# Kernel tuning notes

Measured on AMD Instinct MI355X. Metric: run time of the kernel, lower is better.

Reference implementation:

```python
import jax, jax.numpy as jnp
import numpy as np

L = 16          # n_levels
F = 2           # n_features_per_level
LOG2_T = 19
T = 1 << LOG2_T # hashmap size per level
BASE_RES = 16
FINEST_RES = 2048
_b = (FINEST_RES / BASE_RES) ** (1.0 / (L - 1))
RES = [int(np.floor(BASE_RES * _b ** l)) for l in range(L)]
PRIMES = (1, 2654435761, 805459861, 3674653429)
H = 2 * L * F   # 64 = n_neurons (static 32 + dynamic 32)
N_PTS = 2097152


def hash_encode(coords, table):
    """Multi-resolution hash grid encoding. coords [N,D] in [0,1], table [L,T,F] -> [N, L*F]."""
    N, D = coords.shape
    # 2^D corner offsets of the enclosing grid cell
    offsets = np.stack(
        np.meshgrid(*([np.array([0, 1], dtype=np.uint32)] * D), indexing='ij'), -1
    ).reshape(-1, D)
    primes = [jnp.uint32(p) for p in PRIMES[:D]]
    feats = []
    for l in range(L):  # fixed small loop over levels
        pos = coords * RES[l]
        grid = jnp.floor(pos)
        frac = pos - grid                       # [N,D] interpolation weights
        gu = grid.astype(jnp.int32).astype(jnp.uint32)
        acc = jnp.zeros((N, F), coords.dtype)
        for off in offsets:                     # fixed 2^D corners
            idx = gu + off[None, :]
            h = idx[:, 0] * primes[0]
            for d in range(1, D):
                h = h ^ (idx[:, d] * primes[d])
            h = (h & jnp.uint32(T - 1)).astype(jnp.int32)
            w = jnp.prod(jnp.where(off[None, :] != 0, frac, 1.0 - frac), axis=1)
            acc = acc + w[:, None] * table[l, h]
        feats.append(acc)
    return jnp.concatenate(feats, -1)


def setup_inputs() -> dict:
    key = jax.random.key(0)
    ks = jax.random.split(key, 12)
    s = 1.0 / np.sqrt(H)
    return {
        'x': jax.random.uniform(ks[0], (N_PTS, 3), jnp.float32),
        't': jax.random.uniform(ks[1], (), jnp.float32),
        'table_static': jax.random.uniform(ks[2], (L, T, F), jnp.float32, -1e-4, 1e-4),
        'table_dynamic': jax.random.uniform(ks[3], (L, T, F), jnp.float32, -1e-4, 1e-4),
        'w1_0': jax.random.normal(ks[4], (H, H), jnp.float32) * s,
        'w1_1': jax.random.normal(ks[5], (H, H), jnp.float32) * s,
        'w1_2': jax.random.normal(ks[6], (H, H), jnp.float32) * s,
        'w2_0': jax.random.normal(ks[7], (H, H), jnp.float32) * s,
        'w2_1': jax.random.normal(ks[8], (H, H), jnp.float32) * s,
        'w2_2': jax.random.normal(ks[9], (H, 1), jnp.float32) * s,
        'skip_alpha': jnp.float32(0.5),
    }


def reference(x, t, table_static, table_dynamic, w1_0, w1_1, w1_2,
              w2_0, w2_1, w2_2, skip_alpha):
    relu = jax.nn.relu
    # t_input = cat([x, full((N,1), t)])
    t_col = jnp.broadcast_to(t.astype(x.dtype), (x.shape[0], 1))
    t_input = jnp.concatenate([x, t_col], axis=1)
    static_features = hash_encode(x, table_static)          # [N,32]
    dynamic_features = hash_encode(t_input, table_dynamic)  # [N,32]
    feat = jnp.concatenate([static_features, dynamic_features], -1)  # [N,64]
    # net_1: 2 hidden layers, ReLU everywhere incl. output activation
    h = relu(feat @ w1_0)
    h = relu(h @ w1_1)
    out1 = relu(h @ w1_2)
    # adaptive skip blend
    blend = out1 * skip_alpha + (1.0 - skip_alpha) * feat
    # net_2: 2 hidden layers ReLU, linear output -> [N,1]
    h = relu(blend @ w2_0)
    h = relu(h @ w2_1)
    return h @ w2_2
```

## Files before the change

kernel.cpp:

```cpp
#include <hip/hip_runtime.h>
#include <math.h>

#define LVLS 16
#define TMASK ((1u << 19) - 1u)
#define NT 256
#define TSLICE (1u << 20)
#define KPL (1u << 19)

typedef _Float16 h4 __attribute__((ext_vector_type(4)));
typedef short bf8i __attribute__((ext_vector_type(8)));
typedef float f4 __attribute__((ext_vector_type(4)));

#define ESCALE 1024.0f
#define EINV   0.0009765625f

struct ResParams { float rf[LVLS]; };

__device__ __forceinline__ unsigned hash3(unsigned ux, unsigned uy, unsigned uz) {
    return ux ^ (uy * 2654435761u) ^ (uz * 805459861u);
}

__device__ __forceinline__ unsigned short bf16_rne(float f) {
    unsigned u = __builtin_bit_cast(unsigned, f);
    unsigned r = (u + 0x7FFFu + ((u >> 16) & 1u)) >> 16;
    return (unsigned short)r;
}
__device__ __forceinline__ float bf16_to_f(unsigned short h) {
    unsigned u = ((unsigned)h) << 16;
    return __builtin_bit_cast(float, u);
}
__device__ __forceinline__ void split8(const float* v, bf8i& h, bf8i& l) {
    #pragma unroll
    for (int j = 0; j < 8; ++j) {
        unsigned short hb = bf16_rne(v[j]);
        h[j] = (short)hb;
        l[j] = (short)bf16_rne(v[j] - bf16_to_f(hb));
    }
}

__global__ __launch_bounds__(NT, 8)
void build_E(const float* __restrict__ tabs, const float* __restrict__ tabd,
             const float* __restrict__ t_ptr, h4* __restrict__ E, ResParams rp)
{
    const unsigned idx = blockIdx.x * NT + threadIdx.x;
    const unsigned l = idx >> 19;
    const unsigned k = idx & TMASK;
    const float r = rp.rf[l];
    const float tt = t_ptr[0];
    const float ft = tt * r;
    const float gt = floorf(ft);
    const float wt = ft - gt;
    const unsigned ut = (unsigned)(int)gt;
    const unsigned c0 = (ut * 3674653429u) & TMASK;
    const unsigned c1 = ((ut + 1u) * 3674653429u) & TMASK;
    const float* ts = tabs + (size_t)l * TSLICE;
    const float* td = tabd + (size_t)l * TSLICE;
    const float2 s  = *(const float2*)(ts + (size_t)k * 2u);
    const float2 d0 = *(const float2*)(td + (size_t)(k ^ c0) * 2u);
    const float2 d1 = *(const float2*)(td + (size_t)(k ^ c1) * 2u);
    const float om = 1.f - wt;
    h4 v;
    v.x = (_Float16)(s.x * ESCALE);
    v.y = (_Float16)(s.y * ESCALE);
    v.z = (_Float16)((om * d0.x + wt * d1.x) * ESCALE);
    v.w = (_Float16)((om * d0.y + wt * d1.y) * ESCALE);
    E[idx] = v;
}

__global__ __launch_bounds__(NT)
void build_W(const float* __restrict__ w10, const float* __restrict__ w11,
             const float* __restrict__ w12, const float* __restrict__ w20,
             const float* __restrict__ w21, const float* __restrict__ w22,
             unsigned short* __restrict__ Wf)
{
    const int tid = blockIdx.x * NT + threadIdx.x;
    if (tid >= 6 * 4 * 2 * 64) return;
    const int lane = tid & 63;
    const int ks = (tid >> 6) & 1;
    const int nt = (tid >> 7) & 3;
    const int L  = tid >> 9;
    const int g = lane >> 4, c = lane & 15;
    unsigned short* dst = Wf + (size_t)tid * 16;
    #pragma unroll
    for (int j = 0; j < 8; ++j) {
        const int k = ks * 32 + g * 8 + j;
        float v;
        if      (L == 0) v = w10[k * 64 + nt * 16 + c];
        else if (L == 1) v = w11[k * 64 + nt * 16 + c];
        else if (L == 2) v = w12[k * 64 + nt * 16 + c];
        else if (L == 3) v = w20[k * 64 + nt * 16 + c];
        else if (L == 4) v = w21[k * 64 + nt * 16 + c];
        else             v = (nt == 0 && c == 0) ? w22[k] : 0.f;
        unsigned short hb = bf16_rne(v);
        unsigned short lb = bf16_rne(v - bf16_to_f(hb));
        dst[j]     = hb;
        dst[8 + j] = lb;
    }
}

__global__ __launch_bounds__(NT, 8)
void enc_all(const float* __restrict__ x, const h4* __restrict__ E,
             h4* __restrict__ fb, long cp, int npts, ResParams rp)
{
    const int l = blockIdx.y;
    const int gid = blockIdx.x * NT + threadIdx.x;
    if (gid >= npts) return;
    const float r = rp.rf[l];
    const h4* Es = E + (size_t)l * KPL;

    const float px = x[3 * gid + 0];
    const float py = x[3 * gid + 1];
    const float pz = x[3 * gid + 2];
    const float fx = px * r, fy = py * r, fz = pz * r;
    const float gx = floorf(fx), gy = floorf(fy), gz = floorf(fz);
    const float wx = fx - gx, wy = fy - gy, wz = fz - gz;
    const unsigned ux = (unsigned)(int)gx;
    const unsigned uy = (unsigned)(int)gy;
    const unsigned uz = (unsigned)(int)gz;
    float a0 = 0.f, a1 = 0.f, b0 = 0.f, b1 = 0.f;
    #pragma unroll
    for (int cc = 0; cc < 8; ++cc) {
        const unsigned ox = (cc >> 2) & 1, oy = (cc >> 1) & 1, oz = cc & 1;
        const unsigned kk = hash3(ux + ox, uy + oy, uz + oz) & TMASK;
        const float w = (ox ? wx : 1.f - wx)
                      * (oy ? wy : 1.f - wy)
                      * (oz ? wz : 1.f - wz);
        const h4 e = Es[kk];
        a0 = fmaf(w, (float)e.x, a0);
        a1 = fmaf(w, (float)e.y, a1);
        b0 = fmaf(w, (float)e.z, b0);
        b1 = fmaf(w, (float)e.w, b1);
    }
    h4 v;
    v.x = (_Float16)a0;
    v.y = (_Float16)a1;
    v.z = (_Float16)b0;
    v.w = (_Float16)b1;
    __builtin_nontemporal_store(__builtin_bit_cast(unsigned long long, v),
                                (unsigned long long*)&fb[(size_t)l * cp + gid]);
}

#define MLPT 128
__global__ __launch_bounds__(MLPT)
void mlp_mfma(const h4* __restrict__ fb, long cp, const uint4* __restrict__ Wf,
              const float* __restrict__ alpha_ptr, float* __restrict__ out, int npts)
{
    __shared__ float XBs[2][64 * 68];
    const int lane = threadIdx.x & 63;
    const int wv   = threadIdx.x >> 6;
    const int base = blockIdx.x * MLPT + wv * 64;
    if (base >= npts) return;
    float* xb = XBs[wv];
    const int g = lane >> 4, c = lane & 15;
    const float alpha = alpha_ptr[0];
    const float oma = 1.f - alpha;

    bf8i ah[4][2], al[4][2];

    #pragma unroll
    for (int mt = 0; mt < 4; ++mt) {
        float t0[8], t1[8];
        #pragma unroll
        for (int jj = 0; jj < 4; ++jj) {
            const h4 e = fb[(size_t)(g * 4 + jj) * cp + base + mt * 16 + c];
            t0[2 * jj] = (float)e.x; t0[2 * jj + 1] = (float)e.y;
            t1[2 * jj] = (float)e.z; t1[2 * jj + 1] = (float)e.w;
        }
        split8(t0, ah[mt][0], al[mt][0]);
        split8(t1, ah[mt][1], al[mt][1]);
    }

    auto run_layer = [&](int Lidx, bool relu) {
        #pragma unroll
        for (int nt = 0; nt < 4; ++nt) {
            const uint4* wp0 = Wf + ((size_t)(((Lidx * 4 + nt) * 2 + 0) * 64 + lane)) * 2;
            const uint4* wp1 = Wf + ((size_t)(((Lidx * 4 + nt) * 2 + 1) * 64 + lane)) * 2;
            const bf8i wh0 = __builtin_bit_cast(bf8i, wp0[0]);
            const bf8i wl0 = __builtin_bit_cast(bf8i, wp0[1]);
            const bf8i wh1 = __builtin_bit_cast(bf8i, wp1[0]);
            const bf8i wl1 = __builtin_bit_cast(bf8i, wp1[1]);
            f4 acc[4];
            #pragma unroll
            for (int mt = 0; mt < 4; ++mt) acc[mt] = (f4){0.f, 0.f, 0.f, 0.f};
            #pragma unroll
            for (int mt = 0; mt < 4; ++mt)
                acc[mt] = __builtin_amdgcn_mfma_f32_16x16x32_bf16(ah[mt][0], wh0, acc[mt], 0, 0, 0);
            #pragma unroll
            for (int mt = 0; mt < 4; ++mt)
                acc[mt] = __builtin_amdgcn_mfma_f32_16x16x32_bf16(ah[mt][1], wh1, acc[mt], 0, 0, 0);
            #pragma unroll
            for (int mt = 0; mt < 4; ++mt)
                acc[mt] = __builtin_amdgcn_mfma_f32_16x16x32_bf16(ah[mt][0], wl0, acc[mt], 0, 0, 0);
            #pragma unroll
            for (int mt = 0; mt < 4; ++mt)
                acc[mt] = __builtin_amdgcn_mfma_f32_16x16x32_bf16(ah[mt][1], wl1, acc[mt], 0, 0, 0);
            #pragma unroll
            for (int mt = 0; mt < 4; ++mt)
                acc[mt] = __builtin_amdgcn_mfma_f32_16x16x32_bf16(al[mt][0], wh0, acc[mt], 0, 0, 0);
            #pragma unroll
            for (int mt = 0; mt < 4; ++mt)
                acc[mt] = __builtin_amdgcn_mfma_f32_16x16x32_bf16(al[mt][1], wh1, acc[mt], 0, 0, 0);
            #pragma unroll
            for (int mt = 0; mt < 4; ++mt)
              #pragma unroll
              for (int r = 0; r < 4; ++r) {
                float v = acc[mt][r];
                if (relu) v = fmaxf(v, 0.f);
                xb[(mt * 16 + g * 4 + r) * 68 + nt * 16 + c] = v;
              }
        }
    };

    auto load_frags = [&](bool blend) {
        asm volatile("s_waitcnt lgkmcnt(0)" ::: "memory");
        #pragma unroll
        for (int mt = 0; mt < 4; ++mt) {
            float t0[8], t1[8];
            #pragma unroll
            for (int j = 0; j < 8; ++j) t0[j] = xb[(mt * 16 + c) * 68 + g * 8 + j];
            #pragma unroll
            for (int j = 0; j < 8; ++j) t1[j] = xb[(mt * 16 + c) * 68 + 32 + g * 8 + j];
            if (blend) {
                #pragma unroll
                for (int jj = 0; jj < 4; ++jj) {
                    const h4 e = fb[(size_t)(g * 4 + jj) * cp + base + mt * 16 + c];
                    t0[2 * jj]     = fmaf(t0[2 * jj],     alpha, oma * (float)e.x);
                    t0[2 * jj + 1] = fmaf(t0[2 * jj + 1], alpha, oma * (float)e.y);
                    t1[2 * jj]     = fmaf(t1[2 * jj],     alpha, oma * (float)e.z);
                    t1[2 * jj + 1] = fmaf(t1[2 * jj + 1], alpha, oma * (float)e.w);
                }
            }
            split8(t0, ah[mt][0], al[mt][0]);
            split8(t1, ah[mt][1], al[mt][1]);
        }
        asm volatile("s_waitcnt lgkmcnt(0)" ::: "memory");
    };

    run_layer(0, true);
    load_frags(false);
    run_layer(1, true);
    load_frags(false);
    run_layer(2, true);
    load_frags(true);
    run_layer(3, true);
    load_frags(false);
    run_layer(4, true);
    load_frags(false);

    {
        const uint4* wp0 = Wf + ((size_t)(((5 * 4 + 0) * 2 + 0) * 64 + lane)) * 2;
        const uint4* wp1 = Wf + ((size_t)(((5 * 4 + 0) * 2 + 1) * 64 + lane)) * 2;
        const bf8i wh0 = __builtin_bit_cast(bf8i, wp0[0]);
        const bf8i wl0 = __builtin_bit_cast(bf8i, wp0[1]);
        const bf8i wh1 = __builtin_bit_cast(bf8i, wp1[0]);
        const bf8i wl1 = __builtin_bit_cast(bf8i, wp1[1]);
        f4 acc[4];
        #pragma unroll
        for (int mt = 0; mt < 4; ++mt) acc[mt] = (f4){0.f, 0.f, 0.f, 0.f};
        #pragma unroll
        for (int mt = 0; mt < 4; ++mt)
            acc[mt] = __builtin_amdgcn_mfma_f32_16x16x32_bf16(ah[mt][0], wh0, acc[mt], 0, 0, 0);
        #pragma unroll
        for (int mt = 0; mt < 4; ++mt)
            acc[mt] = __builtin_amdgcn_mfma_f32_16x16x32_bf16(ah[mt][1], wh1, acc[mt], 0, 0, 0);
        #pragma unroll
        for (int mt = 0; mt < 4; ++mt)
            acc[mt] = __builtin_amdgcn_mfma_f32_16x16x32_bf16(ah[mt][0], wl0, acc[mt], 0, 0, 0);
        #pragma unroll
        for (int mt = 0; mt < 4; ++mt)
            acc[mt] = __builtin_amdgcn_mfma_f32_16x16x32_bf16(ah[mt][1], wl1, acc[mt], 0, 0, 0);
        #pragma unroll
        for (int mt = 0; mt < 4; ++mt)
            acc[mt] = __builtin_amdgcn_mfma_f32_16x16x32_bf16(al[mt][0], wh0, acc[mt], 0, 0, 0);
        #pragma unroll
        for (int mt = 0; mt < 4; ++mt)
            acc[mt] = __builtin_amdgcn_mfma_f32_16x16x32_bf16(al[mt][1], wh1, acc[mt], 0, 0, 0);
        if (c == 0) {
            #pragma unroll
            for (int mt = 0; mt < 4; ++mt) {
                float4 st = make_float4(acc[mt][0] * EINV, acc[mt][1] * EINV,
                                        acc[mt][2] * EINV, acc[mt][3] * EINV);
                *reinterpret_cast<float4*>(&out[base + mt * 16 + g * 4]) = st;
            }
        }
    }
}

__global__ __launch_bounds__(NT, 2)
void hashmlp_fused(const float* __restrict__ x, const float* __restrict__ t_ptr,
                   const float* __restrict__ tab_s, const float* __restrict__ tab_d,
                   const float* __restrict__ w10, const float* __restrict__ w11,
                   const float* __restrict__ w12, const float* __restrict__ w20,
                   const float* __restrict__ w21, const float* __restrict__ w22,
                   const float* __restrict__ alpha_ptr, float* __restrict__ out,
                   int n, ResParams rp)
{
    __shared__ float smem[64 * NT];
    const int tid = threadIdx.x;
    const int gid = blockIdx.x * NT + tid;
    if (gid >= n) return;
    const float px = x[3 * gid], py = x[3 * gid + 1], pz = x[3 * gid + 2];
    const float tt = t_ptr[0];
    const float alpha = alpha_ptr[0];
    float feat[64];
    #pragma unroll
    for (int l = 0; l < LVLS; ++l) {
        const float r = rp.rf[l];
        const float fx = px * r, fy = py * r, fz = pz * r;
        const float gx = floorf(fx), gy = floorf(fy), gz = floorf(fz);
        const float wx = fx - gx, wy = fy - gy, wz = fz - gz;
        const unsigned ux = (unsigned)(int)gx, uy = (unsigned)(int)gy, uz = (unsigned)(int)gz;
        const float* tb = tab_s + ((size_t)l << 20);
        float a0 = 0.f, a1 = 0.f;
        #pragma unroll
        for (int cc = 0; cc < 8; ++cc) {
            const unsigned ox = (cc >> 2) & 1, oy = (cc >> 1) & 1, oz = cc & 1;
            const unsigned idx = hash3(ux + ox, uy + oy, uz + oz) & TMASK;
            const float w = (ox ? wx : 1.f - wx) * (oy ? wy : 1.f - wy) * (oz ? wz : 1.f - wz);
            const float2 f = *reinterpret_cast<const float2*>(tb + ((size_t)idx * 2u));
            a0 = fmaf(w, f.x, a0); a1 = fmaf(w, f.y, a1);
        }
        feat[2 * l] = a0; feat[2 * l + 1] = a1;
    }
    #pragma unroll
    for (int l = 0; l < LVLS; ++l) {
        const float r = rp.rf[l];
        const float fx = px * r, fy = py * r, fz = pz * r;
        const float gx = floorf(fx), gy = floorf(fy), gz = floorf(fz);
        const float wx = fx - gx, wy = fy - gy, wz = fz - gz;
        const unsigned ux = (unsigned)(int)gx, uy = (unsigned)(int)gy, uz = (unsigned)(int)gz;
        const float ftp = tt * r;
        const float gt = floorf(ftp);
        const float wtp = ftp - gt;
        const unsigned ut = (unsigned)(int)gt;
        const unsigned ht0 = ut * 3674653429u;
        const unsigned ht1 = (ut + 1u) * 3674653429u;
        const float* tb = tab_d + ((size_t)l << 20);
        float a0 = 0.f, a1 = 0.f;
        #pragma unroll
        for (int cc = 0; cc < 8; ++cc) {
            const unsigned ox = (cc >> 2) & 1, oy = (cc >> 1) & 1, oz = cc & 1;
            const unsigned hs = hash3(ux + ox, uy + oy, uz + oz);
            const float ws = (ox ? wx : 1.f - wx) * (oy ? wy : 1.f - wy) * (oz ? wz : 1.f - wz);
            {
                const unsigned idx = (hs ^ ht0) & TMASK;
                const float w = ws * (1.f - wtp);
                const float2 f = *reinterpret_cast<const float2*>(tb + ((size_t)idx * 2u));
                a0 = fmaf(w, f.x, a0); a1 = fmaf(w, f.y, a1);
            }
            {
                const unsigned idx = (hs ^ ht1) & TMASK;
                const float w = ws * wtp;
                const float2 f = *reinterpret_cast<const float2*>(tb + ((size_t)idx * 2u));
                a0 = fmaf(w, f.x, a0); a1 = fmaf(w, f.y, a1);
            }
        }
        feat[32 + 2 * l] = a0; feat[33 + 2 * l] = a1;
    }
    #pragma unroll
    for (int i = 0; i < 64; ++i) smem[i * NT + tid] = feat[i];
    float acc[64];
    auto layer = [&](const float* __restrict__ W, bool do_relu) {
        #pragma unroll
        for (int j = 0; j < 64; ++j) acc[j] = 0.f;
        for (int i = 0; i < 64; ++i) {
            const float fi = smem[i * NT + tid];
            const float* wr = W + i * 64;
            #pragma unroll
            for (int j = 0; j < 64; ++j) acc[j] = fmaf(fi, wr[j], acc[j]);
        }
        #pragma unroll
        for (int j = 0; j < 64; ++j) {
            const float v = do_relu ? fmaxf(acc[j], 0.f) : acc[j];
            smem[j * NT + tid] = v;
        }
    };
    layer(w10, true); layer(w11, true); layer(w12, true);
    #pragma unroll
    for (int j = 0; j < 64; ++j) {
        const float o1 = smem[j * NT + tid];
        smem[j * NT + tid] = fmaf(o1, alpha, (1.f - alpha) * feat[j]);
    }
    layer(w20, true); layer(w21, true);
    float o = 0.f;
    for (int i = 0; i < 64; ++i) o = fmaf(smem[i * NT + tid], w22[i], o);
    out[gid] = o;
}

extern "C" void kernel_launch(void* const* d_in, const int* in_sizes, int n_in,
                              void* d_out, int out_size, void* d_ws, size_t ws_size,
                              hipStream_t stream) {
    (void)n_in; (void)out_size;
    const float* x     = (const float*)d_in[0];
    const float* t     = (const float*)d_in[1];
    const float* tabs  = (const float*)d_in[2];
    const float* tabd  = (const float*)d_in[3];
    const float* w10   = (const float*)d_in[4];
    const float* w11   = (const float*)d_in[5];
    const float* w12   = (const float*)d_in[6];
    const float* w20   = (const float*)d_in[7];
    const float* w21   = (const float*)d_in[8];
    const float* w22   = (const float*)d_in[9];
    const float* alpha = (const float*)d_in[10];
    float* out = (float*)d_out;
    const int n = in_sizes[0] / 3;

    ResParams rp;
    const double b = pow(2048.0 / 16.0, 1.0 / 15.0);
    for (int l = 0; l < LVLS; ++l)
        rp.rf[l] = (float)(int)floor(16.0 * pow(b, (double)l));

    const size_t E_BYTES = (size_t)LVLS * KPL * 8u;
    const size_t W_BYTES = 128u * 1024u;
    if (ws_size < E_BYTES + W_BYTES + 256u * 1024u) {
        dim3 grid((n + NT - 1) / NT), block(NT);
        hipLaunchKernelGGL(hashmlp_fused, grid, block, 0, stream,
                           x, t, tabs, tabd, w10, w11, w12, w20, w21, w22,
                           alpha, out, n, rp);
        return;
    }

    h4* E = (h4*)d_ws;
    unsigned short* Wf = (unsigned short*)((char*)d_ws + E_BYTES);
    h4* fb = (h4*)((char*)d_ws + E_BYTES + W_BYTES);
    long cp_cap = (long)((ws_size - E_BYTES - W_BYTES) / 128u) & ~255L;
    long cp = cp_cap < (long)n ? cp_cap : (long)n;

    {
        const unsigned total = LVLS * KPL;
        hipLaunchKernelGGL(build_E, dim3(total / NT), dim3(NT), 0, stream,
                           tabs, tabd, t, E, rp);
        hipLaunchKernelGGL(build_W, dim3(12), dim3(NT), 0, stream,
                           w10, w11, w12, w20, w21, w22, Wf);
    }

    for (long start = 0; start < n; start += cp) {
        const long m = (n - start) < cp ? (n - start) : cp;
        dim3 egrid((unsigned)((m + NT - 1) / NT), LVLS);
        hipLaunchKernelGGL(enc_all, egrid, dim3(NT), 0, stream,
                           x + 3 * start, E, fb, cp, (int)m, rp);
        dim3 mgrid((unsigned)((m + MLPT - 1) / MLPT));
        hipLaunchKernelGGL(mlp_mfma, mgrid, dim3(MLPT), 0, stream,
                           fb, cp, (const uint4*)Wf, alpha, out + start, (int)m);
    }
}
```

Before: 1.435 ms.

## Fuse hash encoding into MFMA MLP kernel, drop feature buffer round-trip

Merges the per-level encode kernel into the MLP kernel. Each lane computes the hash-grid features for its own MFMA fragment rows and levels and keeps them in registers for the later skip blend, so the fp16 feature buffer is no longer written to and read back from global memory. It also swizzles the shared-memory staging index to reduce bank conflicts and adds tail guards. The cost is higher register pressure and a single kernel that mixes latency-bound gathers with MFMA work, with less occupancy available to hide gather latency.

```diff
diff --git a/kernel.cpp b/kernel.cpp
--- a/kernel.cpp
+++ b/kernel.cpp
@@ -98,52 +98,11 @@
     }
 }
 
-__global__ __launch_bounds__(NT, 8)
-void enc_all(const float* __restrict__ x, const h4* __restrict__ E,
-             h4* __restrict__ fb, long cp, int npts, ResParams rp)
-{
-    const int l = blockIdx.y;
-    const int gid = blockIdx.x * NT + threadIdx.x;
-    if (gid >= npts) return;
-    const float r = rp.rf[l];
-    const h4* Es = E + (size_t)l * KPL;
-
-    const float px = x[3 * gid + 0];
-    const float py = x[3 * gid + 1];
-    const float pz = x[3 * gid + 2];
-    const float fx = px * r, fy = py * r, fz = pz * r;
-    const float gx = floorf(fx), gy = floorf(fy), gz = floorf(fz);
-    const float wx = fx - gx, wy = fy - gy, wz = fz - gz;
-    const unsigned ux = (unsigned)(int)gx;
-    const unsigned uy = (unsigned)(int)gy;
-    const unsigned uz = (unsigned)(int)gz;
-    float a0 = 0.f, a1 = 0.f, b0 = 0.f, b1 = 0.f;
-    #pragma unroll
-    for (int cc = 0; cc < 8; ++cc) {
-        const unsigned ox = (cc >> 2) & 1, oy = (cc >> 1) & 1, oz = cc & 1;
-        const unsigned kk = hash3(ux + ox, uy + oy, uz + oz) & TMASK;
-        const float w = (ox ? wx : 1.f - wx)
-                      * (oy ? wy : 1.f - wy)
-                      * (oz ? wz : 1.f - wz);
-        const h4 e = Es[kk];
-        a0 = fmaf(w, (float)e.x, a0);
-        a1 = fmaf(w, (float)e.y, a1);
-        b0 = fmaf(w, (float)e.z, b0);
-        b1 = fmaf(w, (float)e.w, b1);
-    }
-    h4 v;
-    v.x = (_Float16)a0;
-    v.y = (_Float16)a1;
-    v.z = (_Float16)b0;
-    v.w = (_Float16)b1;
-    __builtin_nontemporal_store(__builtin_bit_cast(unsigned long long, v),
-                                (unsigned long long*)&fb[(size_t)l * cp + gid]);
-}
-
 #define MLPT 128
-__global__ __launch_bounds__(MLPT)
-void mlp_mfma(const h4* __restrict__ fb, long cp, const uint4* __restrict__ Wf,
-              const float* __restrict__ alpha_ptr, float* __restrict__ out, int npts)
+__global__ __launch_bounds__(MLPT, 2)
+void fused_all(const float* __restrict__ x, const h4* __restrict__ E,
+               const uint4* __restrict__ Wf, const float* __restrict__ alpha_ptr,
+               float* __restrict__ out, int npts, ResParams rp)
 {
     __shared__ float XBs[2][64 * 68];
     const int lane = threadIdx.x & 63;
@@ -155,16 +114,57 @@
     const float alpha = alpha_ptr[0];
     const float oma = 1.f - alpha;
 
+    auto xidx = [](int row, int col6) { return row * 68 + (col6 ^ ((row & 3) << 3)); };
+
+    float rj[4];
+    #pragma unroll
+    for (int jj = 0; jj < 4; ++jj) {
+        const float rlo = (g & 1) ? rp.rf[4 + jj]  : rp.rf[jj];
+        const float rhi = (g & 1) ? rp.rf[12 + jj] : rp.rf[8 + jj];
+        rj[jj] = (g & 2) ? rhi : rlo;
+    }
+
     bf8i ah[4][2], al[4][2];
+    h4 featsave[4][4];
 
     #pragma unroll
     for (int mt = 0; mt < 4; ++mt) {
+        int p = base + mt * 16 + c;
+        if (p >= npts) p = npts - 1;
+        const float px = x[3 * p + 0];
+        const float py = x[3 * p + 1];
+        const float pz = x[3 * p + 2];
         float t0[8], t1[8];
         #pragma unroll
         for (int jj = 0; jj < 4; ++jj) {
-            const h4 e = fb[(size_t)(g * 4 + jj) * cp + base + mt * 16 + c];
-            t0[2 * jj] = (float)e.x; t0[2 * jj + 1] = (float)e.y;
-            t1[2 * jj] = (float)e.z; t1[2 * jj + 1] = (float)e.w;
+            const float r = rj[jj];
+            const unsigned lbase = (unsigned)(g * 4 + jj) << 19;
+            const float fx = px * r, fy = py * r, fz = pz * r;
+            const float gx = floorf(fx), gy = floorf(fy), gz = floorf(fz);
+            const float wx = fx - gx, wy = fy - gy, wz = fz - gz;
+            const unsigned ux = (unsigned)(int)gx;
+            const unsigned uy = (unsigned)(int)gy;
+            const unsigned uz = (unsigned)(int)gz;
+            float a0 = 0.f, a1 = 0.f, b0 = 0.f, b1 = 0.f;
+            #pragma unroll
+            for (int cc = 0; cc < 8; ++cc) {
+                const unsigned ox = (cc >> 2) & 1, oy = (cc >> 1) & 1, oz = cc & 1;
+                const unsigned kk = hash3(ux + ox, uy + oy, uz + oz) & TMASK;
+                const float w = (ox ? wx : 1.f - wx)
+                              * (oy ? wy : 1.f - wy)
+                              * (oz ? wz : 1.f - wz);
+                const h4 e = E[(size_t)(lbase + kk)];
+                a0 = fmaf(w, (float)e.x, a0);
+                a1 = fmaf(w, (float)e.y, a1);
+                b0 = fmaf(w, (float)e.z, b0);
+                b1 = fmaf(w, (float)e.w, b1);
+            }
+            h4 v;
+            v.x = (_Float16)a0; v.y = (_Float16)a1;
+            v.z = (_Float16)b0; v.w = (_Float16)b1;
+            featsave[mt][jj] = v;
+            t0[2 * jj] = (float)v.x; t0[2 * jj + 1] = (float)v.y;
+            t1[2 * jj] = (float)v.z; t1[2 * jj + 1] = (float)v.w;
         }
         split8(t0, ah[mt][0], al[mt][0]);
         split8(t1, ah[mt][1], al[mt][1]);
@@ -206,7 +206,7 @@
               for (int r = 0; r < 4; ++r) {
                 float v = acc[mt][r];
                 if (relu) v = fmaxf(v, 0.f);
-                xb[(mt * 16 + g * 4 + r) * 68 + nt * 16 + c] = v;
+                xb[xidx(mt * 16 + g * 4 + r, nt * 16 + c)] = v;
               }
         }
     };
@@ -217,13 +217,13 @@
         for (int mt = 0; mt < 4; ++mt) {
             float t0[8], t1[8];
             #pragma unroll
-            for (int j = 0; j < 8; ++j) t0[j] = xb[(mt * 16 + c) * 68 + g * 8 + j];
-            #pragma unroll
-            for (int j = 0; j < 8; ++j) t1[j] = xb[(mt * 16 + c) * 68 + 32 + g * 8 + j];
+            for (int j = 0; j < 8; ++j) t0[j] = xb[xidx(mt * 16 + c, g * 8 + j)];
+            #pragma unroll
+            for (int j = 0; j < 8; ++j) t1[j] = xb[xidx(mt * 16 + c, 32 + g * 8 + j)];
             if (blend) {
                 #pragma unroll
                 for (int jj = 0; jj < 4; ++jj) {
-                    const h4 e = fb[(size_t)(g * 4 + jj) * cp + base + mt * 16 + c];
+                    const h4 e = featsave[mt][jj];
                     t0[2 * jj]     = fmaf(t0[2 * jj],     alpha, oma * (float)e.x);
                     t0[2 * jj + 1] = fmaf(t0[2 * jj + 1], alpha, oma * (float)e.y);
                     t1[2 * jj]     = fmaf(t1[2 * jj],     alpha, oma * (float)e.z);
@@ -278,9 +278,16 @@
         if (c == 0) {
             #pragma unroll
             for (int mt = 0; mt < 4; ++mt) {
-                float4 st = make_float4(acc[mt][0] * EINV, acc[mt][1] * EINV,
-                                        acc[mt][2] * EINV, acc[mt][3] * EINV);
-                *reinterpret_cast<float4*>(&out[base + mt * 16 + g * 4]) = st;
+                const int o = base + mt * 16 + g * 4;
+                const float4 st = make_float4(acc[mt][0] * EINV, acc[mt][1] * EINV,
+                                              acc[mt][2] * EINV, acc[mt][3] * EINV);
+                if (o + 4 <= npts) {
+                    *reinterpret_cast<float4*>(&out[o]) = st;
+                } else {
+                    const float sv[4] = {st.x, st.y, st.z, st.w};
+                    for (int k = 0; k < 4; ++k)
+                        if (o + k < npts) out[o + k] = sv[k];
+                }
             }
         }
     }
@@ -412,7 +419,7 @@
 
     const size_t E_BYTES = (size_t)LVLS * KPL * 8u;
     const size_t W_BYTES = 128u * 1024u;
-    if (ws_size < E_BYTES + W_BYTES + 256u * 1024u) {
+    if (ws_size < E_BYTES + W_BYTES) {
         dim3 grid((n + NT - 1) / NT), block(NT);
         hipLaunchKernelGGL(hashmlp_fused, grid, block, 0, stream,
                            x, t, tabs, tabd, w10, w11, w12, w20, w21, w22,
@@ -422,9 +429,6 @@
 
     h4* E = (h4*)d_ws;
     unsigned short* Wf = (unsigned short*)((char*)d_ws + E_BYTES);
-    h4* fb = (h4*)((char*)d_ws + E_BYTES + W_BYTES);
-    long cp_cap = (long)((ws_size - E_BYTES - W_BYTES) / 128u) & ~255L;
-    long cp = cp_cap < (long)n ? cp_cap : (long)n;
 
     {
         const unsigned total = LVLS * KPL;
@@ -434,13 +438,7 @@
                            w10, w11, w12, w20, w21, w22, Wf);
     }
 
-    for (long start = 0; start < n; start += cp) {
-        const long m = (n - start) < cp ? (n - start) : cp;
-        dim3 egrid((unsigned)((m + NT - 1) / NT), LVLS);
-        hipLaunchKernelGGL(enc_all, egrid, dim3(NT), 0, stream,
-                           x + 3 * start, E, fb, cp, (int)m, rp);
-        dim3 mgrid((unsigned)((m + MLPT - 1) / MLPT));
-        hipLaunchKernelGGL(mlp_mfma, mgrid, dim3(MLPT), 0, stream,
-                           fb, cp, (const uint4*)Wf, alpha, out + start, (int)m);
-    }
-}
+    dim3 fgrid((unsigned)((n + MLPT - 1) / MLPT));
+    hipLaunchKernelGGL(fused_all, fgrid, dim3(MLPT), 0, stream,
+                       x, E, (const uint4*)Wf, alpha, out, n, rp);
+}
```

Result: slower. 2.382 ms (+66.0%).

## Interleave encode blocks across levels and truncate bf16 split with packed ops

Applied to the files above, without the earlier changes.

The encode grid becomes one-dimensional, with the level index taken from the low bits of the block id. Consecutive blocks now cover all 16 levels for the same points, which is meant to improve locality of the x reads and spread the hash table traffic across levels. The hi/lo bf16 split for the MLP fragments now truncates instead of rounding to nearest and packs pairs straight into 32-bit words, cutting ALU work. Truncating the hi part still leaves an exact residual in the lo part, so accuracy of the two-term split should stay about the same.

```diff
diff --git a/kernel.cpp b/kernel.cpp
--- a/kernel.cpp
+++ b/kernel.cpp
@@ -29,13 +29,25 @@
     unsigned u = ((unsigned)h) << 16;
     return __builtin_bit_cast(float, u);
 }
-__device__ __forceinline__ void split8(const float* v, bf8i& h, bf8i& l) {
-    #pragma unroll
-    for (int j = 0; j < 8; ++j) {
-        unsigned short hb = bf16_rne(v[j]);
-        h[j] = (short)hb;
-        l[j] = (short)bf16_rne(v[j] - bf16_to_f(hb));
-    }
+
+__device__ __forceinline__ void split8t(const float* v, bf8i& h, bf8i& l) {
+    unsigned H[4], L[4];
+    #pragma unroll
+    for (int p = 0; p < 4; ++p) {
+        const unsigned u0 = __builtin_bit_cast(unsigned, v[2 * p]);
+        const unsigned u1 = __builtin_bit_cast(unsigned, v[2 * p + 1]);
+        const unsigned h0 = u0 & 0xffff0000u;
+        const unsigned h1 = u1 & 0xffff0000u;
+        const float l0 = v[2 * p]     - __builtin_bit_cast(float, h0);
+        const float l1 = v[2 * p + 1] - __builtin_bit_cast(float, h1);
+        H[p] = (u0 >> 16) | h1;
+        L[p] = (__builtin_bit_cast(unsigned, l0) >> 16)
+             | (__builtin_bit_cast(unsigned, l1) & 0xffff0000u);
+    }
+    uint4 Hv = make_uint4(H[0], H[1], H[2], H[3]);
+    uint4 Lv = make_uint4(L[0], L[1], L[2], L[3]);
+    h = __builtin_bit_cast(bf8i, Hv);
+    l = __builtin_bit_cast(bf8i, Lv);
 }
 
 __global__ __launch_bounds__(NT, 8)
@@ -102,8 +114,9 @@
 void enc_all(const float* __restrict__ x, const h4* __restrict__ E,
              h4* __restrict__ fb, long cp, int npts, ResParams rp)
 {
-    const int l = blockIdx.y;
-    const int gid = blockIdx.x * NT + threadIdx.x;
+    const int b = blockIdx.x;
+    const int l = b & 15;
+    const int gid = (b >> 4) * NT + threadIdx.x;
     if (gid >= npts) return;
     const float r = rp.rf[l];
     const h4* Es = E + (size_t)l * KPL;
@@ -166,8 +179,8 @@
             t0[2 * jj] = (float)e.x; t0[2 * jj + 1] = (float)e.y;
             t1[2 * jj] = (float)e.z; t1[2 * jj + 1] = (float)e.w;
         }
-        split8(t0, ah[mt][0], al[mt][0]);
-        split8(t1, ah[mt][1], al[mt][1]);
+        split8t(t0, ah[mt][0], al[mt][0]);
+        split8t(t1, ah[mt][1], al[mt][1]);
     }
 
     auto run_layer = [&](int Lidx, bool relu) {
@@ -230,8 +243,8 @@
                     t1[2 * jj + 1] = fmaf(t1[2 * jj + 1], alpha, oma * (float)e.w);
                 }
             }
-            split8(t0, ah[mt][0], al[mt][0]);
-            split8(t1, ah[mt][1], al[mt][1]);
+            split8t(t0, ah[mt][0], al[mt][0]);
+            split8t(t1, ah[mt][1], al[mt][1]);
         }
         asm volatile("s_waitcnt lgkmcnt(0)" ::: "memory");
     };
@@ -436,8 +449,8 @@
 
     for (long start = 0; start < n; start += cp) {
         const long m = (n - start) < cp ? (n - start) : cp;
-        dim3 egrid((unsigned)((m + NT - 1) / NT), LVLS);
-        hipLaunchKernelGGL(enc_all, egrid, dim3(NT), 0, stream,
+        const unsigned ptb = (unsigned)((m + NT - 1) / NT);
+        hipLaunchKernelGGL(enc_all, dim3(ptb * 16), dim3(NT), 0, stream,
                            x + 3 * start, E, fb, cp, (int)m, rp);
         dim3 mgrid((unsigned)((m + MLPT - 1) / MLPT));
         hipLaunchKernelGGL(mlp_mfma, mgrid, dim3(MLPT), 0, stream,
```

Result: slower. 1.673 ms (+16.6%).
